# Optimization experiments

Hardware: AMD Instinct MI355X
Metric: run time of the kernel (lower is better)

Reference implementation:

```python
import jax, jax.numpy as jnp
import numpy as np

N_EXPERTS = 8
TOPK = 2
W_IMPORTANCE = 0.01
W_LOAD = 0.01
LAMBDA_Z = 0.001
W_PENALTY = 0.01
PENALTY_TEMP = 1.66


def setup_inputs() -> dict:
    key = jax.random.key(0)
    ks = jax.random.split(key, 8)
    B, S, D, H, E = 8, 4096, 512, 2048, N_EXPERTS
    T = B * S
    return {
        "x": jax.random.normal(ks[0], (B, S, D), dtype=jnp.float32),
        "gate_w": jax.random.normal(ks[1], (E, D), dtype=jnp.float32) * 0.02,
        "noise_w": jax.random.normal(ks[2], (E, D), dtype=jnp.float32) * 0.02,
        "bias": jnp.zeros((E,), dtype=jnp.float32),
        "c_fc_w": jax.random.normal(ks[3], (E, H, D), dtype=jnp.float32) * 0.02,
        "c_fc_b": jnp.zeros((E, H), dtype=jnp.float32),
        "c_proj_w": jax.random.normal(ks[4], (E, D, H), dtype=jnp.float32) * 0.02,
        "c_proj_b": jnp.zeros((E, D), dtype=jnp.float32),
        "noise": jax.random.normal(ks[5], (T, E), dtype=jnp.float32),
    }


def reference(x, gate_w, noise_w, bias, c_fc_w, c_fc_b, c_proj_w, c_proj_b, noise):
    E, K = N_EXPERTS, TOPK
    D = x.shape[-1]
    xs = x.reshape(-1, D)                      # [T, D]
    T = xs.shape[0]

    gate_logits = xs @ gate_w.T                # [T, E]

    # penalty (pre-noise logits)
    p = jax.nn.softmax(gate_logits / PENALTY_TEMP, axis=-1)
    penalty_a = jnp.mean(p * (1.0 - p))
    pm = p.mean(axis=0)
    penalty_b = 1.0 / E - jnp.mean(pm * (1.0 - pm))
    penalty = (penalty_a + penalty_b) * W_PENALTY

    # z-loss (pre-noise logits)
    lse = jax.scipy.special.logsumexp(gate_logits, axis=-1)
    z_loss = LAMBDA_Z * jnp.mean(lse ** 2)

    # noisy gating + bias
    noise_std = jax.nn.softplus(xs @ noise_w.T)
    gate_logits = gate_logits + noise * noise_std + bias

    weights_vals, selected = jax.lax.top_k(gate_logits, K)   # [T, K]
    weights = jax.nn.softmax(weights_vals.astype(jnp.float32), axis=1).astype(x.dtype)

    # importance loss: scatter-add weights per expert
    importance = jax.ops.segment_sum(weights.reshape(-1), selected.reshape(-1),
                                     num_segments=E)
    cv2 = jnp.var(importance) / jnp.mean(importance) ** 2
    importance_loss = W_IMPORTANCE * cv2

    # load loss: top-1 counts vs mean router probs (post-noise)
    router_probs = jax.nn.softmax(gate_logits.astype(jnp.float32), axis=-1).astype(x.dtype)
    top1 = selected[:, 0]
    fi = jax.ops.segment_sum(jnp.ones((T,), dtype=jnp.float32), top1,
                             num_segments=E) / T
    load_loss = W_LOAD * E * jnp.sum(fi * router_probs.mean(axis=0))

    aux = penalty + z_loss + importance_loss + load_loss

    # combine weights per (token, expert): [T, E]
    comb = jnp.zeros((T, E), dtype=x.dtype).at[jnp.arange(T)[:, None], selected].add(weights)

    results = jnp.zeros_like(xs)
    for e in range(E):  # fixed small expert count
        h = jax.nn.gelu(xs @ c_fc_w[e].T + c_fc_b[e], approximate=True)
        o = h @ c_proj_w[e].T + c_proj_b[e]
        results = results + comb[:, e:e + 1] * o

    return results.reshape(x.shape), aux
```

## Files before the change

### kernel.cpp

```cpp
#include <hip/hip_runtime.h>
#include <hip/hip_bf16.h>
#include <stdint.h>

#define TTOK 32768
#define DDIM 512
#define HDIM 2048
#define NEXP 8
#define GBLK 1024
#define SBLK 128
#define IDXS (TTOK + 256)

typedef __attribute__((ext_vector_type(4))) float f32x4;
typedef __attribute__((ext_vector_type(8))) short bf16x8;

#define GLOAD16(gp, lp)                                                      \
  __builtin_amdgcn_global_load_lds(                                          \
      (const __attribute__((address_space(1))) unsigned int*)(gp),           \
      (__attribute__((address_space(3))) unsigned int*)(lp), 16, 0, 0)

__device__ __forceinline__ ushort f2bf(float f) {
  union { float f; uint32_t u; } cv; cv.f = f;
  uint32_t u = cv.u;
  u = u + 0x7fffu + ((u >> 16) & 1u);
  return (ushort)(u >> 16);
}

__device__ __forceinline__ float bf2f(ushort u) {
  union { uint32_t u; float f; } cv; cv.u = ((uint32_t)u) << 16;
  return cv.f;
}

__device__ __forceinline__ float gelu_fast(float v) {
  float y = 1.5957691216057308f * (v + 0.044715f * v * v * v);
  return v / (1.0f + __expf(-y));
}

__global__ __launch_bounds__(256) void cvtw_kernel(const float* __restrict__ src,
                                                   ushort* __restrict__ dst, int n4) {
  int i = blockIdx.x * blockDim.x + threadIdx.x;
  if (i >= n4) return;
  float4 v = reinterpret_cast<const float4*>(src)[i];
  ushort4 o;
  o.x = f2bf(v.x); o.y = f2bf(v.y); o.z = f2bf(v.z); o.w = f2bf(v.w);
  reinterpret_cast<ushort4*>(dst)[i] = o;
}

__global__ __launch_bounds__(256, 2) void gating1_kernel(
    const float* __restrict__ x, const float* __restrict__ gw,
    const float* __restrict__ nw, ushort* __restrict__ xbf,
    float* __restrict__ logits) {
  const int tid = threadIdx.x;
  const int lane = tid & 63;
  const int wave = tid >> 6;

  float wg[NEXP][8], wn[NEXP][8];
#pragma unroll
  for (int e = 0; e < NEXP; ++e) {
    const float4* pg = reinterpret_cast<const float4*>(gw + e * DDIM + lane * 8);
    float4 g0 = pg[0], g1 = pg[1];
    wg[e][0] = g0.x; wg[e][1] = g0.y; wg[e][2] = g0.z; wg[e][3] = g0.w;
    wg[e][4] = g1.x; wg[e][5] = g1.y; wg[e][6] = g1.z; wg[e][7] = g1.w;
    const float4* pq = reinterpret_cast<const float4*>(nw + e * DDIM + lane * 8);
    float4 n0 = pq[0], n1 = pq[1];
    wn[e][0] = n0.x; wn[e][1] = n0.y; wn[e][2] = n0.z; wn[e][3] = n0.w;
    wn[e][4] = n1.x; wn[e][5] = n1.y; wn[e][6] = n1.z; wn[e][7] = n1.w;
  }

  const int t00 = blockIdx.x * 32 + wave * 8;
  for (int it = 0; it < 8; it += 2) {
    float xv[2][8];
#pragma unroll
    for (int u = 0; u < 2; ++u) {
      const int t = t00 + it + u;
      const float4* xp = reinterpret_cast<const float4*>(x + (size_t)t * DDIM + lane * 8);
      float4 x0 = xp[0], x1 = xp[1];
      xv[u][0] = x0.x; xv[u][1] = x0.y; xv[u][2] = x0.z; xv[u][3] = x0.w;
      xv[u][4] = x1.x; xv[u][5] = x1.y; xv[u][6] = x1.z; xv[u][7] = x1.w;
      ushort u8[8];
#pragma unroll
      for (int j = 0; j < 8; ++j) u8[j] = f2bf(xv[u][j]);
      uint4 pack;
      pack.x = (uint32_t)u8[0] | ((uint32_t)u8[1] << 16);
      pack.y = (uint32_t)u8[2] | ((uint32_t)u8[3] << 16);
      pack.z = (uint32_t)u8[4] | ((uint32_t)u8[5] << 16);
      pack.w = (uint32_t)u8[6] | ((uint32_t)u8[7] << 16);
      *reinterpret_cast<uint4*>(xbf + (size_t)t * DDIM + lane * 8) = pack;
    }

    float pg[2][NEXP], pn[2][NEXP];
#pragma unroll
    for (int u = 0; u < 2; ++u)
#pragma unroll
      for (int e = 0; e < NEXP; ++e) { pg[u][e] = 0.f; pn[u][e] = 0.f; }
#pragma unroll
    for (int e = 0; e < NEXP; ++e)
#pragma unroll
      for (int j = 0; j < 8; ++j) {
#pragma unroll
        for (int u = 0; u < 2; ++u) {
          pg[u][e] = fmaf(xv[u][j], wg[e][j], pg[u][e]);
          pn[u][e] = fmaf(xv[u][j], wn[e][j], pn[u][e]);
        }
      }
#pragma unroll
    for (int m = 1; m < 64; m <<= 1) {
#pragma unroll
      for (int u = 0; u < 2; ++u)
#pragma unroll
        for (int e = 0; e < NEXP; ++e) {
          pg[u][e] += __shfl_xor(pg[u][e], m);
          pn[u][e] += __shfl_xor(pn[u][e], m);
        }
    }
    if (lane == 0) {
#pragma unroll
      for (int u = 0; u < 2; ++u) {
        const int t = t00 + it + u;
        float4* lp = reinterpret_cast<float4*>(logits + (size_t)t * 16);
        lp[0] = make_float4(pg[u][0], pg[u][1], pg[u][2], pg[u][3]);
        lp[1] = make_float4(pg[u][4], pg[u][5], pg[u][6], pg[u][7]);
        lp[2] = make_float4(pn[u][0], pn[u][1], pn[u][2], pn[u][3]);
        lp[3] = make_float4(pn[u][4], pn[u][5], pn[u][6], pn[u][7]);
      }
    }
  }
}

__global__ void gating2_kernel(
    const float* __restrict__ logits, const float* __restrict__ noise,
    const float* __restrict__ bias, int* __restrict__ cnt,
    int* __restrict__ idxl, int2* __restrict__ slots,
    float2* __restrict__ tokw, float* __restrict__ part) {
  const int tid = threadIdx.x;
  const int lane = tid & 63, wave = tid >> 6;
  const int t = blockIdx.x * 256 + tid;

  const float4* lp = reinterpret_cast<const float4*>(logits + (size_t)t * 16);
  float4 l0 = lp[0], l1 = lp[1], l2 = lp[2], l3 = lp[3];
  float lg[NEXP] = {l0.x, l0.y, l0.z, l0.w, l1.x, l1.y, l1.z, l1.w};
  float nl[NEXP] = {l2.x, l2.y, l2.z, l2.w, l3.x, l3.y, l3.z, l3.w};
  const float4* np = reinterpret_cast<const float4*>(noise + (size_t)t * NEXP);
  float4 z0 = np[0], z1 = np[1];
  float nz[NEXP] = {z0.x, z0.y, z0.z, z0.w, z1.x, z1.y, z1.z, z1.w};
  float bia[NEXP];
#pragma unroll
  for (int e = 0; e < NEXP; ++e) bia[e] = bias[e];

  float pa = 0.f, pm[NEXP];
  {
    float sv[NEXP];
#pragma unroll
    for (int e = 0; e < NEXP; ++e) sv[e] = lg[e] * (1.0f / 1.66f);
    float mx = sv[0];
#pragma unroll
    for (int e = 1; e < NEXP; ++e) mx = fmaxf(mx, sv[e]);
    float ssum = 0.f, pv[NEXP];
#pragma unroll
    for (int e = 0; e < NEXP; ++e) { pv[e] = __expf(sv[e] - mx); ssum += pv[e]; }
    float sinv = 1.f / ssum;
#pragma unroll
    for (int e = 0; e < NEXP; ++e) {
      float pe = pv[e] * sinv;
      pa += pe * (1.f - pe);
      pm[e] = pe;
    }
  }
  float z2;
  {
    float mg = lg[0];
#pragma unroll
    for (int e = 1; e < NEXP; ++e) mg = fmaxf(mg, lg[e]);
    float es = 0.f;
#pragma unroll
    for (int e = 0; e < NEXP; ++e) es += __expf(lg[e] - mg);
    float lse = mg + __logf(es);
    z2 = lse * lse;
  }
  float g2[NEXP];
#pragma unroll
  for (int e = 0; e < NEXP; ++e) {
    float s = nl[e];
    float sp = fmaxf(s, 0.f) + __logf(1.f + __expf(-fabsf(s)));
    g2[e] = lg[e] + nz[e] * sp + bia[e];
  }
  float v1 = g2[0]; int i1 = 0;
#pragma unroll
  for (int e = 1; e < NEXP; ++e) if (g2[e] > v1) { v1 = g2[e]; i1 = e; }
  float v2 = -3.4e38f; int i2 = 0;
#pragma unroll
  for (int e = 0; e < NEXP; ++e) if (e != i1 && g2[e] > v2) { v2 = g2[e]; i2 = e; }
  float dd = __expf(v2 - v1);
  float w1 = 1.f / (1.f + dd);
  float w2 = dd / (1.f + dd);
  float rp[NEXP];
  {
    float mr = g2[0];
#pragma unroll
    for (int e = 1; e < NEXP; ++e) mr = fmaxf(mr, g2[e]);
    float rs = 0.f, er[NEXP];
#pragma unroll
    for (int e = 0; e < NEXP; ++e) { er[e] = __expf(g2[e] - mr); rs += er[e]; }
    float rinv = 1.f / rs;
#pragma unroll
    for (int e = 0; e < NEXP; ++e) rp[e] = er[e] * rinv;
  }

  float loc[34];
  loc[0] = pa; loc[1] = z2;
#pragma unroll
  for (int e = 0; e < NEXP; ++e) {
    loc[2 + e]  = pm[e];
    loc[10 + e] = (e == i1 ? w1 : 0.f) + (e == i2 ? w2 : 0.f);
    loc[18 + e] = rp[e];
    loc[26 + e] = (e == i1) ? 1.f : 0.f;
  }
#pragma unroll
  for (int m = 1; m < 64; m <<= 1) {
#pragma unroll
    for (int s = 0; s < 34; ++s) loc[s] += __shfl_xor(loc[s], m);
  }
  __shared__ float red[4][34];
  if (lane == 0) {
#pragma unroll
    for (int s = 0; s < 34; ++s) red[wave][s] = loc[s];
  }
  __shared__ int lcnt[NEXP], gbase[NEXP];
  if (tid < NEXP) lcnt[tid] = 0;
  __syncthreads();
  int p1 = atomicAdd(&lcnt[i1], 1);
  int p2 = atomicAdd(&lcnt[i2], 1);
  __syncthreads();
  if (tid < NEXP) gbase[tid] = atomicAdd(&cnt[tid], lcnt[tid]);
  if (tid < 34) {
    float s = red[0][tid] + red[1][tid] + red[2][tid] + red[3][tid];
    part[(size_t)tid * SBLK + blockIdx.x] = s;
  }
  __syncthreads();
  int q1 = gbase[i1] + p1, q2 = gbase[i2] + p2;
  idxl[i1 * IDXS + q1] = t;
  idxl[i2 * IDXS + q2] = t;
  slots[t] = make_int2((i1 << 16) | q1, (i2 << 16) | q2);
  tokw[t] = make_float2(w1, w2);
}

__global__ __launch_bounds__(256) void finalize_kernel(
    const float* __restrict__ part, const int* __restrict__ cnt,
    int* __restrict__ offs, int* __restrict__ idxl,
    float* __restrict__ aux_out) {
  __shared__ float sums[34];
  __shared__ float red[4][34];
  __shared__ int roundc[NEXP], base[NEXP];
  const int tid = threadIdx.x;
  const int lane = tid & 63, wave = tid >> 6;

  float loc[34];
#pragma unroll
  for (int s = 0; s < 34; ++s) loc[s] = 0.f;
  for (int b = tid; b < SBLK; b += 256) {
#pragma unroll
    for (int s = 0; s < 34; ++s) loc[s] += part[(size_t)s * SBLK + b];
  }
#pragma unroll
  for (int m = 1; m < 64; m <<= 1) {
#pragma unroll
    for (int s = 0; s < 34; ++s) loc[s] += __shfl_xor(loc[s], m);
  }
  if (lane == 0) {
#pragma unroll
    for (int s = 0; s < 34; ++s) red[wave][s] = loc[s];
  }
  if (tid == 0) {
    int acc = 0;
    for (int e = 0; e < NEXP; ++e) {
      int r = (cnt[e] + 255) & ~255;
      roundc[e] = r; base[e] = acc; acc += r;
    }
  }
  __syncthreads();
  if (tid < 34) sums[tid] = red[0][tid] + red[1][tid] + red[2][tid] + red[3][tid];
  __syncthreads();
  for (int i = tid; i < NEXP * 256; i += 256) {
    int e = i >> 8, k = i & 255;
    int pos = cnt[e] + k;
    if (pos < roundc[e]) idxl[e * IDXS + pos] = 0;
  }
  if (tid < NEXP) offs[tid] = base[tid];
  if (tid == 0) {
    const float Tf = (float)TTOK;
    float pa = sums[0] / (Tf * 8.f);
    float pbm = 0.f;
    for (int e = 0; e < NEXP; ++e) { float pm = sums[2 + e] / Tf; pbm += pm * (1.f - pm); }
    float pb = 1.f / 8.f - pbm / 8.f;
    float penalty = (pa + pb) * 0.01f;
    float z = 0.001f * sums[1] / Tf;
    float mean = 0.f;
    for (int e = 0; e < NEXP; ++e) mean += sums[10 + e];
    mean /= 8.f;
    float var = 0.f;
    for (int e = 0; e < NEXP; ++e) { float d = sums[10 + e] - mean; var += d * d; }
    var /= 8.f;
    float il = 0.01f * var / (mean * mean);
    float ld = 0.f;
    for (int e = 0; e < NEXP; ++e) ld += (sums[26 + e] / Tf) * (sums[18 + e] / Tf);
    ld *= 0.01f * 8.f;
    aux_out[0] = penalty + z + il + ld;
  }
}


__global__ __launch_bounds__(512, 4) void gemm1_kernel(
    const ushort* __restrict__ xbf, const ushort* __restrict__ wfc,
    const float* __restrict__ fcb, const int* __restrict__ idxl,
    const int* __restrict__ cnt, const int* __restrict__ offs,
    ushort* __restrict__ h, int hbase, int HC) {
  const int e = blockIdx.z;
  const int count = cnt[e];
  const int rounded = (count + 255) & ~255;
  const int mt = blockIdx.x;
  if (mt * 256 >= rounded) return;
  const int nt = blockIdx.y;
  const int tid = threadIdx.x;
  const int lane = tid & 63, wave = tid >> 6;
  const int wm = wave >> 1, wn = wave & 1;

  __shared__ ushort As[256][64];
  __shared__ ushort Bs[128][64];

  const int srow = tid >> 3;
  const int csw8 = (((tid & 7) ^ (srow & 7)) << 3);
  const int dst8 = ((tid & 7) << 3);

  int gA[4];
  const ushort* bbase = wfc + (size_t)e * (HDIM * DDIM) +
                        (size_t)(hbase + nt * 128) * DDIM;
#pragma unroll
  for (int r = 0; r < 4; ++r)
    gA[r] = idxl[e * IDXS + mt * 256 + srow + r * 64];

  f32x4 acc[4][4];
#pragma unroll
  for (int m = 0; m < 4; ++m)
#pragma unroll
    for (int n = 0; n < 4; ++n)
      acc[m][n] = (f32x4){0.f, 0.f, 0.f, 0.f};

  const int NK = DDIM / 64;
  for (int kt = 0; kt < NK; ++kt) {
    const int koff = kt * 64;
#pragma unroll
    for (int r = 0; r < 4; ++r)
      GLOAD16(xbf + (size_t)gA[r] * DDIM + koff + csw8, &As[srow + r * 64][dst8]);
#pragma unroll
    for (int r = 0; r < 2; ++r)
      GLOAD16(bbase + (size_t)(srow + r * 64) * DDIM + koff + csw8, &Bs[srow + r * 64][dst8]);
    asm volatile("s_waitcnt vmcnt(0)" ::: "memory");
    __syncthreads();
#pragma unroll
    for (int ks = 0; ks < 2; ++ks) {
      const int ch = (((ks << 2) | (lane >> 4)) ^ (lane & 7)) << 3;
      bf16x8 af[4], bfr[4];
#pragma unroll
      for (int m = 0; m < 4; ++m)
        af[m] = *reinterpret_cast<const bf16x8*>(&As[wm * 64 + m * 16 + (lane & 15)][ch]);
#pragma unroll
      for (int n = 0; n < 4; ++n)
        bfr[n] = *reinterpret_cast<const bf16x8*>(&Bs[wn * 64 + n * 16 + (lane & 15)][ch]);
#pragma unroll
      for (int m = 0; m < 4; ++m)
#pragma unroll
        for (int n = 0; n < 4; ++n)
          acc[m][n] = __builtin_amdgcn_mfma_f32_16x16x32_bf16(af[m], bfr[n], acc[m][n], 0, 0, 0);
    }
    __syncthreads();
  }

  const int hb = offs[e];
#pragma unroll
  for (int n = 0; n < 4; ++n) {
    const int col = wn * 64 + n * 16 + (lane & 15);
    const int gcol = hbase + nt * 128 + col;
    const float bterm = fcb[e * HDIM + gcol];
#pragma unroll
    for (int m = 0; m < 4; ++m) {
#pragma unroll
      for (int j = 0; j < 4; ++j) {
        const int row = mt * 256 + wm * 64 + m * 16 + ((lane >> 4) << 2) + j;
        float v = acc[m][n][j] + bterm;
        h[(size_t)(hb + row) * HC + (nt * 128 + col)] = f2bf(gelu_fast(v));
      }
    }
  }
}

__global__ __launch_bounds__(512, 4) void gemm2_kernel(
    const ushort* __restrict__ h, const ushort* __restrict__ wpj,
    const float* __restrict__ pjb, const int* __restrict__ cnt,
    const int* __restrict__ offs, ushort* __restrict__ scratch,
    int hbase, int HC, int first_chunk) {
  const int e = blockIdx.z;
  const int count = cnt[e];
  const int rounded = (count + 255) & ~255;
  const int mt = blockIdx.x;
  if (mt * 256 >= rounded) return;
  const int nt = blockIdx.y;
  const int tid = threadIdx.x;
  const int lane = tid & 63, wave = tid >> 6;
  const int wm = wave >> 1, wn = wave & 1;

  __shared__ ushort As[256][64];
  __shared__ ushort Bs[128][64];

  const int srow = tid >> 3;
  const int csw8 = (((tid & 7) ^ (srow & 7)) << 3);
  const int dst8 = ((tid & 7) << 3);
  const int hb = offs[e];

  const ushort* abase = h + (size_t)(hb + mt * 256) * HC;
  const ushort* bbase = wpj + (size_t)e * (DDIM * HDIM) +
                        (size_t)(nt * 128) * HDIM + hbase;

  f32x4 acc[4][4];
#pragma unroll
  for (int m = 0; m < 4; ++m)
#pragma unroll
    for (int n = 0; n < 4; ++n)
      acc[m][n] = (f32x4){0.f, 0.f, 0.f, 0.f};

  const int NK = HC / 64;
  for (int kt = 0; kt < NK; ++kt) {
    const int koff = kt * 64;
#pragma unroll
    for (int r = 0; r < 4; ++r)
      GLOAD16(abase + (size_t)(srow + r * 64) * HC + koff + csw8, &As[srow + r * 64][dst8]);
#pragma unroll
    for (int r = 0; r < 2; ++r)
      GLOAD16(bbase + (size_t)(srow + r * 64) * HDIM + koff + csw8, &Bs[srow + r * 64][dst8]);
    asm volatile("s_waitcnt vmcnt(0)" ::: "memory");
    __syncthreads();
#pragma unroll
    for (int ks = 0; ks < 2; ++ks) {
      const int ch = (((ks << 2) | (lane >> 4)) ^ (lane & 7)) << 3;
      bf16x8 af[4], bfr[4];
#pragma unroll
      for (int m = 0; m < 4; ++m)
        af[m] = *reinterpret_cast<const bf16x8*>(&As[wm * 64 + m * 16 + (lane & 15)][ch]);
#pragma unroll
      for (int n = 0; n < 4; ++n)
        bfr[n] = *reinterpret_cast<const bf16x8*>(&Bs[wn * 64 + n * 16 + (lane & 15)][ch]);
#pragma unroll
      for (int m = 0; m < 4; ++m)
#pragma unroll
        for (int n = 0; n < 4; ++n)
          acc[m][n] = __builtin_amdgcn_mfma_f32_16x16x32_bf16(af[m], bfr[n], acc[m][n], 0, 0, 0);
    }
    __syncthreads();
  }

#pragma unroll
  for (int n = 0; n < 4; ++n) {
    const int col = nt * 128 + wn * 64 + n * 16 + (lane & 15);
    const float bterm = pjb[e * DDIM + col];
#pragma unroll
    for (int m = 0; m < 4; ++m) {
#pragma unroll
      for (int j = 0; j < 4; ++j) {
        const size_t row = (size_t)(hb + mt * 256 + wm * 64 + m * 16 + ((lane >> 4) << 2) + j);
        ushort* p = scratch + row * DDIM + col;
        float v = acc[m][n][j];
        if (first_chunk) v += bterm;
        else v += bf2f(*p);
        *p = f2bf(v);
      }
    }
  }
}

__global__ __launch_bounds__(256, 8) void combine_kernel(
    const ushort* __restrict__ scratch, const int* __restrict__ offs,
    const int2* __restrict__ slots, const float2* __restrict__ tokw,
    float* __restrict__ out) {
  const int lane = threadIdx.x & 63;
  const int wave = threadIdx.x >> 6;
  const int t = blockIdx.x * 4 + wave;
  int2 s = slots[t];
  float2 w = tokw[t];
  const int r1 = offs[s.x >> 16] + (s.x & 0xFFFF);
  const int r2 = offs[s.y >> 16] + (s.y & 0xFFFF);
  bf16x8 a = *reinterpret_cast<const bf16x8*>(scratch + (size_t)r1 * DDIM + lane * 8);
  bf16x8 b = *reinterpret_cast<const bf16x8*>(scratch + (size_t)r2 * DDIM + lane * 8);
  float r[8];
#pragma unroll
  for (int j = 0; j < 8; ++j)
    r[j] = w.x * bf2f((ushort)a[j]) + w.y * bf2f((ushort)b[j]);
  float4* op = reinterpret_cast<float4*>(out + (size_t)t * DDIM + lane * 8);
  op[0] = make_float4(r[0], r[1], r[2], r[3]);
  op[1] = make_float4(r[4], r[5], r[6], r[7]);
}

extern "C" void kernel_launch(void* const* d_in, const int* in_sizes, int n_in,
                              void* d_out, int out_size, void* d_ws, size_t ws_size,
                              hipStream_t stream) {
  const float* x    = (const float*)d_in[0];
  const float* gw   = (const float*)d_in[1];
  const float* nw   = (const float*)d_in[2];
  const float* bias = (const float*)d_in[3];
  const float* fcw  = (const float*)d_in[4];
  const float* fcb  = (const float*)d_in[5];
  const float* pjw  = (const float*)d_in[6];
  const float* pjb  = (const float*)d_in[7];
  const float* noise = (const float*)d_in[8];
  float* out = (float*)d_out;

  char* ws = (char*)d_ws;
  size_t o = 0;
  auto alloc = [&](size_t bytes) -> char* {
    char* p = ws + o;
    o += (bytes + 255) & ~(size_t)255;
    return p;
  };
  ushort* xbf    = (ushort*)alloc((size_t)TTOK * DDIM * 2);
  ushort* wfcb   = (ushort*)alloc((size_t)NEXP * HDIM * DDIM * 2);
  ushort* wpjb   = (ushort*)alloc((size_t)NEXP * DDIM * HDIM * 2);
  float*  logits = (float*)alloc((size_t)TTOK * 16 * 4);
  int*    idxl   = (int*)alloc((size_t)NEXP * IDXS * 4);
  int2*   slots  = (int2*)alloc((size_t)TTOK * 8);
  float2* tokw   = (float2*)alloc((size_t)TTOK * 8);
  int*    cnt    = (int*)alloc(256);
  int*    offs   = (int*)alloc(256);
  float*  part   = (float*)alloc(34 * SBLK * 4);
  ushort* scr    = (ushort*)alloc((size_t)(2 * TTOK + 2048) * DDIM * 2);
  size_t fixed = o;

  int NCH = 16;
  const int chs[5] = {1, 2, 4, 8, 16};
  for (int ci = 0; ci < 5; ++ci) {
    size_t need = fixed + (size_t)(2 * TTOK + 2048) * (size_t)(HDIM / chs[ci]) * 2;
    if (need <= ws_size) { NCH = chs[ci]; break; }
  }
  const int HC = HDIM / NCH;
  ushort* h = (ushort*)alloc((size_t)(2 * TTOK + 2048) * HC * 2);

  hipMemsetAsync(cnt, 0, 32, stream);

  cvtw_kernel<<<8192, 256, 0, stream>>>(fcw, wfcb, NEXP * HDIM * DDIM / 4);
  cvtw_kernel<<<8192, 256, 0, stream>>>(pjw, wpjb, NEXP * DDIM * HDIM / 4);
  gating1_kernel<<<GBLK, 256, 0, stream>>>(x, gw, nw, xbf, logits);
  gating2_kernel<<<SBLK, 256, 0, stream>>>(logits, noise, bias, cnt, idxl, slots, tokw, part);
  finalize_kernel<<<1, 256, 0, stream>>>(part, cnt, offs, idxl, out + ((size_t)out_size - 1));

  for (int c = 0; c < NCH; ++c) {
    gemm1_kernel<<<dim3(128, HC / 128, NEXP), 512, 0, stream>>>(
        xbf, wfcb, fcb, idxl, cnt, offs, h, c * HC, HC);
    gemm2_kernel<<<dim3(128, 4, NEXP), 512, 0, stream>>>(
        h, wpjb, pjb, cnt, offs, scr, c * HC, HC, c == 0);
  }
  combine_kernel<<<TTOK / 4, 256, 0, stream>>>(scr, offs, slots, tokw, out);
}
```

Baseline: 691.8 us.

## Double-buffer GEMM LDS tiles and restage gating logits through shared memory

The two expert GEMM kernels now use two LDS buffers, prefetching the next K-tile with global_load_lds while MFMAs run on the current one. A partial vmcnt wait replaces the full drain before each barrier. The gating kernel is rewritten to stage 16 tokens and the 16 gate/noise weight rows in shared memory and compute one dot product per thread, which removes the 6-step shuffle reductions. Doubling LDS to 96KB per GEMM block may lower occupancy, and the gating LDS reads may hit bank conflicts.

```diff
diff --git a/kernel.cpp b/kernel.cpp
--- a/kernel.cpp
+++ b/kernel.cpp
@@ -6,7 +6,6 @@
 #define DDIM 512
 #define HDIM 2048
 #define NEXP 8
-#define GBLK 1024
 #define SBLK 128
 #define IDXS (TTOK + 256)
 
@@ -49,81 +48,45 @@
     const float* __restrict__ x, const float* __restrict__ gw,
     const float* __restrict__ nw, ushort* __restrict__ xbf,
     float* __restrict__ logits) {
+  __shared__ float xs[16][516];
+  __shared__ float wsm[16][516];
   const int tid = threadIdx.x;
-  const int lane = tid & 63;
-  const int wave = tid >> 6;
-
-  float wg[NEXP][8], wn[NEXP][8];
-#pragma unroll
-  for (int e = 0; e < NEXP; ++e) {
-    const float4* pg = reinterpret_cast<const float4*>(gw + e * DDIM + lane * 8);
-    float4 g0 = pg[0], g1 = pg[1];
-    wg[e][0] = g0.x; wg[e][1] = g0.y; wg[e][2] = g0.z; wg[e][3] = g0.w;
-    wg[e][4] = g1.x; wg[e][5] = g1.y; wg[e][6] = g1.z; wg[e][7] = g1.w;
-    const float4* pq = reinterpret_cast<const float4*>(nw + e * DDIM + lane * 8);
-    float4 n0 = pq[0], n1 = pq[1];
-    wn[e][0] = n0.x; wn[e][1] = n0.y; wn[e][2] = n0.z; wn[e][3] = n0.w;
-    wn[e][4] = n1.x; wn[e][5] = n1.y; wn[e][6] = n1.z; wn[e][7] = n1.w;
-  }
-
-  const int t00 = blockIdx.x * 32 + wave * 8;
-  for (int it = 0; it < 8; it += 2) {
-    float xv[2][8];
-#pragma unroll
-    for (int u = 0; u < 2; ++u) {
-      const int t = t00 + it + u;
-      const float4* xp = reinterpret_cast<const float4*>(x + (size_t)t * DDIM + lane * 8);
-      float4 x0 = xp[0], x1 = xp[1];
-      xv[u][0] = x0.x; xv[u][1] = x0.y; xv[u][2] = x0.z; xv[u][3] = x0.w;
-      xv[u][4] = x1.x; xv[u][5] = x1.y; xv[u][6] = x1.z; xv[u][7] = x1.w;
-      ushort u8[8];
-#pragma unroll
-      for (int j = 0; j < 8; ++j) u8[j] = f2bf(xv[u][j]);
-      uint4 pack;
-      pack.x = (uint32_t)u8[0] | ((uint32_t)u8[1] << 16);
-      pack.y = (uint32_t)u8[2] | ((uint32_t)u8[3] << 16);
-      pack.z = (uint32_t)u8[4] | ((uint32_t)u8[5] << 16);
-      pack.w = (uint32_t)u8[6] | ((uint32_t)u8[7] << 16);
-      *reinterpret_cast<uint4*>(xbf + (size_t)t * DDIM + lane * 8) = pack;
-    }
-
-    float pg[2][NEXP], pn[2][NEXP];
-#pragma unroll
-    for (int u = 0; u < 2; ++u)
-#pragma unroll
-      for (int e = 0; e < NEXP; ++e) { pg[u][e] = 0.f; pn[u][e] = 0.f; }
-#pragma unroll
-    for (int e = 0; e < NEXP; ++e)
-#pragma unroll
-      for (int j = 0; j < 8; ++j) {
-#pragma unroll
-        for (int u = 0; u < 2; ++u) {
-          pg[u][e] = fmaf(xv[u][j], wg[e][j], pg[u][e]);
-          pn[u][e] = fmaf(xv[u][j], wn[e][j], pn[u][e]);
-        }
-      }
-#pragma unroll
-    for (int m = 1; m < 64; m <<= 1) {
-#pragma unroll
-      for (int u = 0; u < 2; ++u)
-#pragma unroll
-        for (int e = 0; e < NEXP; ++e) {
-          pg[u][e] += __shfl_xor(pg[u][e], m);
-          pn[u][e] += __shfl_xor(pn[u][e], m);
-        }
-    }
-    if (lane == 0) {
-#pragma unroll
-      for (int u = 0; u < 2; ++u) {
-        const int t = t00 + it + u;
-        float4* lp = reinterpret_cast<float4*>(logits + (size_t)t * 16);
-        lp[0] = make_float4(pg[u][0], pg[u][1], pg[u][2], pg[u][3]);
-        lp[1] = make_float4(pg[u][4], pg[u][5], pg[u][6], pg[u][7]);
-        lp[2] = make_float4(pn[u][0], pn[u][1], pn[u][2], pn[u][3]);
-        lp[3] = make_float4(pn[u][4], pn[u][5], pn[u][6], pn[u][7]);
-      }
-    }
-  }
+  const int t0 = blockIdx.x * 16;
+
+  for (int i = tid; i < 2048; i += 256) {
+    int row = i >> 7;
+    int d4 = (i & 127) << 2;
+    const float* src = (row < 8) ? (gw + row * DDIM + d4)
+                                 : (nw + (row - 8) * DDIM + d4);
+    *reinterpret_cast<float4*>(&wsm[row][d4]) =
+        *reinterpret_cast<const float4*>(src);
+  }
+  for (int i = tid; i < 2048; i += 256) {
+    int row = i >> 7;
+    int d4 = (i & 127) << 2;
+    float4 v = *reinterpret_cast<const float4*>(x + (size_t)(t0 + row) * DDIM + d4);
+    *reinterpret_cast<float4*>(&xs[row][d4]) = v;
+    ushort4 u;
+    u.x = f2bf(v.x); u.y = f2bf(v.y); u.z = f2bf(v.z); u.w = f2bf(v.w);
+    *reinterpret_cast<ushort4*>(xbf + (size_t)(t0 + row) * DDIM + d4) = u;
+  }
+  __syncthreads();
+
+  const int unit = tid & 15;
+  const int tok = tid >> 4;
+  const float* xr = &xs[tok][0];
+  const float* wr = &wsm[unit][0];
+  float a0 = 0.f, a1 = 0.f, a2 = 0.f, a3 = 0.f;
+#pragma unroll 16
+  for (int d = 0; d < 512; d += 4) {
+    float4 xv = *reinterpret_cast<const float4*>(xr + d);
+    float4 wv = *reinterpret_cast<const float4*>(wr + d);
+    a0 = fmaf(xv.x, wv.x, a0);
+    a1 = fmaf(xv.y, wv.y, a1);
+    a2 = fmaf(xv.z, wv.z, a2);
+    a3 = fmaf(xv.w, wv.w, a3);
+  }
+  logits[(size_t)(t0 + tok) * 16 + unit] = (a0 + a1) + (a2 + a3);
 }
 
 __global__ void gating2_kernel(
@@ -308,6 +271,36 @@
 }
 
 
+#define GEMM_PIPE(STAGE_MACRO, NK_)                                           \
+  STAGE_MACRO(0, 0);                                                          \
+  for (int kt = 0; kt < (NK_); ++kt) {                                        \
+    const int cur = kt & 1;                                                   \
+    if (kt + 1 < (NK_)) {                                                     \
+      STAGE_MACRO(cur ^ 1, kt + 1);                                           \
+      asm volatile("s_waitcnt vmcnt(6)" ::: "memory");                        \
+    } else {                                                                  \
+      asm volatile("s_waitcnt vmcnt(0)" ::: "memory");                        \
+    }                                                                         \
+    __builtin_amdgcn_s_barrier();                                             \
+    __builtin_amdgcn_sched_barrier(0);                                        \
+    _Pragma("unroll") for (int ks = 0; ks < 2; ++ks) {                        \
+      const int ch = (((ks << 2) | (lane >> 4)) ^ (lane & 7)) << 3;           \
+      bf16x8 af[4], bfr[4];                                                   \
+      _Pragma("unroll") for (int m = 0; m < 4; ++m)                           \
+        af[m] = *reinterpret_cast<const bf16x8*>(                             \
+            &As[cur][wm * 64 + m * 16 + (lane & 15)][ch]);                    \
+      _Pragma("unroll") for (int n = 0; n < 4; ++n)                           \
+        bfr[n] = *reinterpret_cast<const bf16x8*>(                            \
+            &Bs[cur][wn * 64 + n * 16 + (lane & 15)][ch]);                    \
+      _Pragma("unroll") for (int m = 0; m < 4; ++m)                           \
+        _Pragma("unroll") for (int n = 0; n < 4; ++n)                         \
+          acc[m][n] = __builtin_amdgcn_mfma_f32_16x16x32_bf16(                \
+              af[m], bfr[n], acc[m][n], 0, 0, 0);                             \
+    }                                                                         \
+    __builtin_amdgcn_sched_barrier(0);                                        \
+    __builtin_amdgcn_s_barrier();                                             \
+  }
+
 __global__ __launch_bounds__(512, 4) void gemm1_kernel(
     const ushort* __restrict__ xbf, const ushort* __restrict__ wfc,
     const float* __restrict__ fcb, const int* __restrict__ idxl,
@@ -323,8 +316,8 @@
   const int lane = tid & 63, wave = tid >> 6;
   const int wm = wave >> 1, wn = wave & 1;
 
-  __shared__ ushort As[256][64];
-  __shared__ ushort Bs[128][64];
+  __shared__ ushort As[2][256][64];
+  __shared__ ushort Bs[2][128][64];
 
   const int srow = tid >> 3;
   const int csw8 = (((tid & 7) ^ (srow & 7)) << 3);
@@ -344,35 +337,18 @@
     for (int n = 0; n < 4; ++n)
       acc[m][n] = (f32x4){0.f, 0.f, 0.f, 0.f};
 
-  const int NK = DDIM / 64;
-  for (int kt = 0; kt < NK; ++kt) {
-    const int koff = kt * 64;
-#pragma unroll
-    for (int r = 0; r < 4; ++r)
-      GLOAD16(xbf + (size_t)gA[r] * DDIM + koff + csw8, &As[srow + r * 64][dst8]);
-#pragma unroll
-    for (int r = 0; r < 2; ++r)
-      GLOAD16(bbase + (size_t)(srow + r * 64) * DDIM + koff + csw8, &Bs[srow + r * 64][dst8]);
-    asm volatile("s_waitcnt vmcnt(0)" ::: "memory");
-    __syncthreads();
-#pragma unroll
-    for (int ks = 0; ks < 2; ++ks) {
-      const int ch = (((ks << 2) | (lane >> 4)) ^ (lane & 7)) << 3;
-      bf16x8 af[4], bfr[4];
-#pragma unroll
-      for (int m = 0; m < 4; ++m)
-        af[m] = *reinterpret_cast<const bf16x8*>(&As[wm * 64 + m * 16 + (lane & 15)][ch]);
-#pragma unroll
-      for (int n = 0; n < 4; ++n)
-        bfr[n] = *reinterpret_cast<const bf16x8*>(&Bs[wn * 64 + n * 16 + (lane & 15)][ch]);
-#pragma unroll
-      for (int m = 0; m < 4; ++m)
-#pragma unroll
-        for (int n = 0; n < 4; ++n)
-          acc[m][n] = __builtin_amdgcn_mfma_f32_16x16x32_bf16(af[m], bfr[n], acc[m][n], 0, 0, 0);
-    }
-    __syncthreads();
-  }
+#define G1_STAGE(buf, kt)                                                     \
+  {                                                                           \
+    const int koff = (kt) * 64;                                               \
+    _Pragma("unroll") for (int r = 0; r < 4; ++r)                             \
+      GLOAD16(xbf + (size_t)gA[r] * DDIM + koff + csw8,                       \
+              &As[buf][srow + r * 64][dst8]);                                 \
+    _Pragma("unroll") for (int r = 0; r < 2; ++r)                             \
+      GLOAD16(bbase + (size_t)(srow + r * 64) * DDIM + koff + csw8,           \
+              &Bs[buf][srow + r * 64][dst8]);                                 \
+  }
+
+  GEMM_PIPE(G1_STAGE, DDIM / 64)
 
   const int hb = offs[e];
 #pragma unroll
@@ -407,8 +383,8 @@
   const int lane = tid & 63, wave = tid >> 6;
   const int wm = wave >> 1, wn = wave & 1;
 
-  __shared__ ushort As[256][64];
-  __shared__ ushort Bs[128][64];
+  __shared__ ushort As[2][256][64];
+  __shared__ ushort Bs[2][128][64];
 
   const int srow = tid >> 3;
   const int csw8 = (((tid & 7) ^ (srow & 7)) << 3);
@@ -426,35 +402,18 @@
     for (int n = 0; n < 4; ++n)
       acc[m][n] = (f32x4){0.f, 0.f, 0.f, 0.f};
 
-  const int NK = HC / 64;
-  for (int kt = 0; kt < NK; ++kt) {
-    const int koff = kt * 64;
-#pragma unroll
-    for (int r = 0; r < 4; ++r)
-      GLOAD16(abase + (size_t)(srow + r * 64) * HC + koff + csw8, &As[srow + r * 64][dst8]);
-#pragma unroll
-    for (int r = 0; r < 2; ++r)
-      GLOAD16(bbase + (size_t)(srow + r * 64) * HDIM + koff + csw8, &Bs[srow + r * 64][dst8]);
-    asm volatile("s_waitcnt vmcnt(0)" ::: "memory");
-    __syncthreads();
-#pragma unroll
-    for (int ks = 0; ks < 2; ++ks) {
-      const int ch = (((ks << 2) | (lane >> 4)) ^ (lane & 7)) << 3;
-      bf16x8 af[4], bfr[4];
-#pragma unroll
-      for (int m = 0; m < 4; ++m)
-        af[m] = *reinterpret_cast<const bf16x8*>(&As[wm * 64 + m * 16 + (lane & 15)][ch]);
-#pragma unroll
-      for (int n = 0; n < 4; ++n)
-        bfr[n] = *reinterpret_cast<const bf16x8*>(&Bs[wn * 64 + n * 16 + (lane & 15)][ch]);
-#pragma unroll
-      for (int m = 0; m < 4; ++m)
-#pragma unroll
-        for (int n = 0; n < 4; ++n)
-          acc[m][n] = __builtin_amdgcn_mfma_f32_16x16x32_bf16(af[m], bfr[n], acc[m][n], 0, 0, 0);
-    }
-    __syncthreads();
-  }
+#define G2_STAGE(buf, kt)                                                     \
+  {                                                                           \
+    const int koff = (kt) * 64;                                               \
+    _Pragma("unroll") for (int r = 0; r < 4; ++r)                             \
+      GLOAD16(abase + (size_t)(srow + r * 64) * HC + koff + csw8,             \
+              &As[buf][srow + r * 64][dst8]);                                 \
+    _Pragma("unroll") for (int r = 0; r < 2; ++r)                             \
+      GLOAD16(bbase + (size_t)(srow + r * 64) * HDIM + koff + csw8,           \
+              &Bs[buf][srow + r * 64][dst8]);                                 \
+  }
+
+  GEMM_PIPE(G2_STAGE, HC / 64)
 
 #pragma unroll
   for (int n = 0; n < 4; ++n) {
@@ -544,7 +503,7 @@
 
   cvtw_kernel<<<8192, 256, 0, stream>>>(fcw, wfcb, NEXP * HDIM * DDIM / 4);
   cvtw_kernel<<<8192, 256, 0, stream>>>(pjw, wpjb, NEXP * DDIM * HDIM / 4);
-  gating1_kernel<<<GBLK, 256, 0, stream>>>(x, gw, nw, xbf, logits);
+  gating1_kernel<<<TTOK / 16, 256, 0, stream>>>(x, gw, nw, xbf, logits);
   gating2_kernel<<<SBLK, 256, 0, stream>>>(logits, noise, bias, cnt, idxl, slots, tokw, part);
   finalize_kernel<<<1, 256, 0, stream>>>(part, cnt, offs, idxl, out + ((size_t)out_size - 1));
 
```

Result: slower. 953.1 us (+37.8%).

## Restructure gating logits kernel to stage tokens and weights in shared memory

Applied to the files above, without the earlier changes.

The gating kernel now loads 16 tokens and all 16 gate/noise weight rows into padded LDS tiles, and each thread computes one (token, unit) dot product over the full dimension. This replaces the old per-wave approach, which kept weights in registers and did a 64-lane shuffle reduction for every token. The aim is to remove the shuffle-reduction overhead and register pressure. In exchange, every block reloads the weights from global memory and uses about 66KB of LDS, which may limit occupancy.

```diff
diff --git a/kernel.cpp b/kernel.cpp
--- a/kernel.cpp
+++ b/kernel.cpp
@@ -6,7 +6,6 @@
 #define DDIM 512
 #define HDIM 2048
 #define NEXP 8
-#define GBLK 1024
 #define SBLK 128
 #define IDXS (TTOK + 256)
 
@@ -49,81 +48,45 @@
     const float* __restrict__ x, const float* __restrict__ gw,
     const float* __restrict__ nw, ushort* __restrict__ xbf,
     float* __restrict__ logits) {
+  __shared__ float xs[16][516];
+  __shared__ float wsm[16][516];
   const int tid = threadIdx.x;
-  const int lane = tid & 63;
-  const int wave = tid >> 6;
-
-  float wg[NEXP][8], wn[NEXP][8];
-#pragma unroll
-  for (int e = 0; e < NEXP; ++e) {
-    const float4* pg = reinterpret_cast<const float4*>(gw + e * DDIM + lane * 8);
-    float4 g0 = pg[0], g1 = pg[1];
-    wg[e][0] = g0.x; wg[e][1] = g0.y; wg[e][2] = g0.z; wg[e][3] = g0.w;
-    wg[e][4] = g1.x; wg[e][5] = g1.y; wg[e][6] = g1.z; wg[e][7] = g1.w;
-    const float4* pq = reinterpret_cast<const float4*>(nw + e * DDIM + lane * 8);
-    float4 n0 = pq[0], n1 = pq[1];
-    wn[e][0] = n0.x; wn[e][1] = n0.y; wn[e][2] = n0.z; wn[e][3] = n0.w;
-    wn[e][4] = n1.x; wn[e][5] = n1.y; wn[e][6] = n1.z; wn[e][7] = n1.w;
-  }
-
-  const int t00 = blockIdx.x * 32 + wave * 8;
-  for (int it = 0; it < 8; it += 2) {
-    float xv[2][8];
-#pragma unroll
-    for (int u = 0; u < 2; ++u) {
-      const int t = t00 + it + u;
-      const float4* xp = reinterpret_cast<const float4*>(x + (size_t)t * DDIM + lane * 8);
-      float4 x0 = xp[0], x1 = xp[1];
-      xv[u][0] = x0.x; xv[u][1] = x0.y; xv[u][2] = x0.z; xv[u][3] = x0.w;
-      xv[u][4] = x1.x; xv[u][5] = x1.y; xv[u][6] = x1.z; xv[u][7] = x1.w;
-      ushort u8[8];
-#pragma unroll
-      for (int j = 0; j < 8; ++j) u8[j] = f2bf(xv[u][j]);
-      uint4 pack;
-      pack.x = (uint32_t)u8[0] | ((uint32_t)u8[1] << 16);
-      pack.y = (uint32_t)u8[2] | ((uint32_t)u8[3] << 16);
-      pack.z = (uint32_t)u8[4] | ((uint32_t)u8[5] << 16);
-      pack.w = (uint32_t)u8[6] | ((uint32_t)u8[7] << 16);
-      *reinterpret_cast<uint4*>(xbf + (size_t)t * DDIM + lane * 8) = pack;
-    }
-
-    float pg[2][NEXP], pn[2][NEXP];
-#pragma unroll
-    for (int u = 0; u < 2; ++u)
-#pragma unroll
-      for (int e = 0; e < NEXP; ++e) { pg[u][e] = 0.f; pn[u][e] = 0.f; }
-#pragma unroll
-    for (int e = 0; e < NEXP; ++e)
-#pragma unroll
-      for (int j = 0; j < 8; ++j) {
-#pragma unroll
-        for (int u = 0; u < 2; ++u) {
-          pg[u][e] = fmaf(xv[u][j], wg[e][j], pg[u][e]);
-          pn[u][e] = fmaf(xv[u][j], wn[e][j], pn[u][e]);
-        }
-      }
-#pragma unroll
-    for (int m = 1; m < 64; m <<= 1) {
-#pragma unroll
-      for (int u = 0; u < 2; ++u)
-#pragma unroll
-        for (int e = 0; e < NEXP; ++e) {
-          pg[u][e] += __shfl_xor(pg[u][e], m);
-          pn[u][e] += __shfl_xor(pn[u][e], m);
-        }
-    }
-    if (lane == 0) {
-#pragma unroll
-      for (int u = 0; u < 2; ++u) {
-        const int t = t00 + it + u;
-        float4* lp = reinterpret_cast<float4*>(logits + (size_t)t * 16);
-        lp[0] = make_float4(pg[u][0], pg[u][1], pg[u][2], pg[u][3]);
-        lp[1] = make_float4(pg[u][4], pg[u][5], pg[u][6], pg[u][7]);
-        lp[2] = make_float4(pn[u][0], pn[u][1], pn[u][2], pn[u][3]);
-        lp[3] = make_float4(pn[u][4], pn[u][5], pn[u][6], pn[u][7]);
-      }
-    }
-  }
+  const int t0 = blockIdx.x * 16;
+
+  for (int i = tid; i < 2048; i += 256) {
+    int row = i >> 7;
+    int d4 = (i & 127) << 2;
+    const float* src = (row < 8) ? (gw + row * DDIM + d4)
+                                 : (nw + (row - 8) * DDIM + d4);
+    *reinterpret_cast<float4*>(&wsm[row][d4]) =
+        *reinterpret_cast<const float4*>(src);
+  }
+  for (int i = tid; i < 2048; i += 256) {
+    int row = i >> 7;
+    int d4 = (i & 127) << 2;
+    float4 v = *reinterpret_cast<const float4*>(x + (size_t)(t0 + row) * DDIM + d4);
+    *reinterpret_cast<float4*>(&xs[row][d4]) = v;
+    ushort4 u;
+    u.x = f2bf(v.x); u.y = f2bf(v.y); u.z = f2bf(v.z); u.w = f2bf(v.w);
+    *reinterpret_cast<ushort4*>(xbf + (size_t)(t0 + row) * DDIM + d4) = u;
+  }
+  __syncthreads();
+
+  const int unit = tid & 15;
+  const int tok = tid >> 4;
+  const float* xr = &xs[tok][0];
+  const float* wr = &wsm[unit][0];
+  float a0 = 0.f, a1 = 0.f, a2 = 0.f, a3 = 0.f;
+#pragma unroll 16
+  for (int d = 0; d < 512; d += 4) {
+    float4 xv = *reinterpret_cast<const float4*>(xr + d);
+    float4 wv = *reinterpret_cast<const float4*>(wr + d);
+    a0 = fmaf(xv.x, wv.x, a0);
+    a1 = fmaf(xv.y, wv.y, a1);
+    a2 = fmaf(xv.z, wv.z, a2);
+    a3 = fmaf(xv.w, wv.w, a3);
+  }
+  logits[(size_t)(t0 + tok) * 16 + unit] = (a0 + a1) + (a2 + a3);
 }
 
 __global__ void gating2_kernel(
@@ -544,7 +507,7 @@
 
   cvtw_kernel<<<8192, 256, 0, stream>>>(fcw, wfcb, NEXP * HDIM * DDIM / 4);
   cvtw_kernel<<<8192, 256, 0, stream>>>(pjw, wpjb, NEXP * DDIM * HDIM / 4);
-  gating1_kernel<<<GBLK, 256, 0, stream>>>(x, gw, nw, xbf, logits);
+  gating1_kernel<<<TTOK / 16, 256, 0, stream>>>(x, gw, nw, xbf, logits);
   gating2_kernel<<<SBLK, 256, 0, stream>>>(logits, noise, bias, cnt, idxl, slots, tokw, part);
   finalize_kernel<<<1, 256, 0, stream>>>(part, cnt, offs, idxl, out + ((size_t)out_size - 1));
 
```

Result: no change. 699.2 us (+1.1%).
